# Performance work log

Hardware: AMD Instinct MI355X
Metric: run time of the kernel (lower is better)

Reference implementation:

```python
import jax, jax.numpy as jnp
import numpy as np

CAD = 5          # cubes_around_atoms_dim (default)
RES = 1.0        # resolution (default)
SIGMA = 0.93     # gaussian sigma from Li et al. 2014
LATO = 2 * CAD + 1


def _cube_offsets():
    # (LATO^3, 3) integer offsets of the neighborhood cube, as float32
    g = jnp.arange(-CAD, CAD + 1, dtype=jnp.float32)
    return jnp.stack(jnp.meshgrid(g, g, g, indexing='ij'), axis=-1).reshape(-1, 3)


def _compute_boxsize(coords):
    # Mirrors the torch code's data-dependent box sizing (concrete values).
    c = np.asarray(coords)
    minm = np.trunc(c.min(axis=1) / RES).min(axis=0)   # (3,)
    maxc = c.reshape(-1, 3).max(axis=0)                # (3,)
    return tuple(int(np.ceil(maxc[d] / RES) - minm[d] + (2 * CAD + 1)) for d in range(3))


def _forward(coords, radius, channels, numberchannels, boxsize):
    B, N, _ = coords.shape
    cube = _cube_offsets()                                   # (K,3), K = LATO^3
    mincoords = jnp.trunc(jnp.min(coords, axis=1) / RES)     # (B,3)
    translation = (mincoords - CAD)[:, None, :]              # (B,1,3)
    coords_s = coords * (1.0 / RES) - translation            # (B,N,3) scaled coords
    radius_s = radius * (1.0 / RES)                          # (B,N)
    # torch uses coords_scaled.data -> detached discrete coordinates
    disc = jnp.trunc(jax.lax.stop_gradient(coords_s))        # (B,N,3)
    # voxel centers: disc + cube + 1 + 0.5*resolution
    centers = disc[:, :, None, :] + cube[None, None] + (1.0 + 0.5 * RES)  # (B,N,K,3)
    dist = jnp.linalg.norm(coords_s[:, :, None, :] - centers, axis=-1)    # (B,N,K)
    expo = -(dist ** 2) / (SIGMA ** 2 * radius_s[:, :, None] ** 2)
    # torch clamps exponent at 10 via masked_fill (never hit: expo <= 0)
    occ = jnp.exp(jnp.minimum(expo, 10.0))                   # (B,N,K)
    idx = (disc[:, :, None, :] + cube[None, None] + 1.0).astype(jnp.int32)  # (B,N,K,3)
    b_idx = jnp.broadcast_to(jnp.arange(B, dtype=jnp.int32)[:, None, None], occ.shape)
    c_idx = jnp.broadcast_to(channels[:, :, None].astype(jnp.int32), occ.shape)
    vol = jnp.zeros((B, numberchannels) + boxsize, dtype=coords.dtype)
    vol = vol.at[b_idx.ravel(), c_idx.ravel(),
                 idx[..., 0].ravel(), idx[..., 1].ravel(), idx[..., 2].ravel()].add(occ.ravel())
    return vol


def setup_inputs() -> dict:
    key = jax.random.key(0)
    k1, k2, k3 = jax.random.split(key, 3)
    B, N, C = 4, 6000, 8
    coords = jax.random.uniform(k1, (B, N, 3), dtype=jnp.float32) * 60.0   # Angstrom box
    radius = 1.2 + 0.8 * jax.random.uniform(k2, (B, N), dtype=jnp.float32)  # vdW-like radii
    channels = jax.random.randint(k3, (B, N), 0, C)
    return {"coords": coords, "radius": radius, "channels": channels, "numberchannels": C}


def reference(coords, radius, channels, numberchannels):
    boxsize = _compute_boxsize(coords)
    return _forward(coords, radius, channels, numberchannels, boxsize)
```

## Files before the change

### kernel.cpp

```cpp
#include <hip/hip_runtime.h>


#define CAD 5
#define LATO 11
#define KOFF 1331
#define SIGMA 0.93f
#define BFIX 4
#define CFIX 8

#define RX 8
#define RY 8
#define RZ 8
#define XSTR 65
#define XCH_C (8 * XSTR)
#define STAGE 256
#define NBB_CAP 8192

#define WS_MIN   0
#define WS_MAX   12
#define WS_OFFS  48
#define WS_PACK  (WS_OFFS + BFIX * NBB_CAP + 64)

struct Geo {
    int bx, by, bz, nbx, nby, nbz, nbb, nrx, nry, nrz;
    float tr[BFIX][3];
};

__device__ __forceinline__ void derive_geo(const float* __restrict__ ws, Geo& g) {
    float box[3];
#pragma unroll
    for (int d = 0; d < 3; ++d) {
        float lo = 1e30f, hi = -1e30f;
#pragma unroll
        for (int b = 0; b < BFIX; ++b) {
            float mnb = truncf(ws[WS_MIN + b * 3 + d]);
            lo = fminf(lo, mnb);
            hi = fmaxf(hi, ws[WS_MAX + b * 3 + d]);
            g.tr[b][d] = mnb - (float)CAD;
        }
        box[d] = ceilf(hi) - lo + (float)(2 * CAD + 1);
    }
    g.bx = (int)box[0]; g.by = (int)box[1]; g.bz = (int)box[2];
    g.nbx = (g.bx + 3) >> 2; g.nby = (g.by + 3) >> 2; g.nbz = (g.bz + 3) >> 2;
    g.nbb = g.nbx * g.nby * g.nbz;
    g.nrx = (g.bx + RX - 1) / RX;
    g.nry = (g.by + RY - 1) / RY;
    g.nrz = (g.bz + RZ - 1) / RZ;
}

__global__ __launch_bounds__(256) void vx_minmax(const float* __restrict__ coords,
                                                 int N, float* __restrict__ ws) {
    int b = blockIdx.x;
    const float* c = coords + (size_t)b * N * 3;
    float mn[3] = {1e30f, 1e30f, 1e30f};
    float mx[3] = {-1e30f, -1e30f, -1e30f};
    for (int i = threadIdx.x; i < N; i += 256) {
#pragma unroll
        for (int d = 0; d < 3; ++d) {
            float v = c[i * 3 + d];
            mn[d] = fminf(mn[d], v);
            mx[d] = fmaxf(mx[d], v);
        }
    }
#pragma unroll
    for (int off = 32; off >= 1; off >>= 1) {
#pragma unroll
        for (int d = 0; d < 3; ++d) {
            mn[d] = fminf(mn[d], __shfl_down(mn[d], off, 64));
            mx[d] = fmaxf(mx[d], __shfl_down(mx[d], off, 64));
        }
    }
    __shared__ float smn[4][3], smx[4][3];
    int wave = threadIdx.x >> 6;
    if ((threadIdx.x & 63) == 0) {
#pragma unroll
        for (int d = 0; d < 3; ++d) { smn[wave][d] = mn[d]; smx[wave][d] = mx[d]; }
    }
    __syncthreads();
    if (threadIdx.x == 0) {
#pragma unroll
        for (int d = 0; d < 3; ++d) {
            for (int w = 1; w < 4; ++w) {
                mn[d] = fminf(mn[d], smn[w][d]);
                mx[d] = fmaxf(mx[d], smx[w][d]);
            }
            ws[WS_MIN + b * 3 + d] = mn[d];
            ws[WS_MAX + b * 3 + d] = mx[d];
        }
    }
}

__global__ __launch_bounds__(1024) void vx_bin(const float* __restrict__ coords,
                                               const float* __restrict__ radius,
                                               const int* __restrict__ channels,
                                               float* __restrict__ ws, int N) {
    int b = blockIdx.x;
    Geo g;
    derive_geo(ws, g);
    int* wsI = (int*)ws;
    int nbb = g.nbb;
    int t = threadIdx.x;

    __shared__ int cnt[NBB_CAP];
    __shared__ int ssum[1024];

    for (int i = t; i < nbb; i += 1024) cnt[i] = 0;
    __syncthreads();

    const float* cb = coords + (size_t)b * N * 3;
    float trx = g.tr[b][0], try_ = g.tr[b][1], trz = g.tr[b][2];

    for (int i = t; i < N; i += 1024) {
        float sx = cb[i * 3 + 0] - trx;
        float sy = cb[i * 3 + 1] - try_;
        float sz = cb[i * 3 + 2] - trz;
        int bin = ((((int)sx) >> 2) * g.nby + (((int)sy) >> 2)) * g.nbz + (((int)sz) >> 2);
        atomicAdd(&cnt[bin], 1);
    }
    __syncthreads();

    int base = t * 8;
    int v[8];
    int sum = 0;
#pragma unroll
    for (int k = 0; k < 8; ++k) {
        v[k] = sum;
        int idx = base + k;
        sum += (idx < nbb) ? cnt[idx] : 0;
    }
    ssum[t] = sum;
    __syncthreads();
    for (int off = 1; off < 1024; off <<= 1) {
        int x = (t >= off) ? ssum[t - off] : 0;
        __syncthreads();
        ssum[t] += x;
        __syncthreads();
    }
    int excl = ssum[t] - sum;
    int gbase = b * N;
#pragma unroll
    for (int k = 0; k < 8; ++k) {
        int idx = base + k;
        if (idx < nbb) {
            int off = gbase + excl + v[k];
            wsI[WS_OFFS + b * nbb + idx] = off;
        }
    }
    __syncthreads();
#pragma unroll
    for (int k = 0; k < 8; ++k) {
        int idx = base + k;
        if (idx < nbb) cnt[idx] = gbase + excl + v[k];
    }
    if (b == BFIX - 1 && t == 0) wsI[WS_OFFS + BFIX * nbb] = BFIX * N;
    __syncthreads();

    float4* p4 = (float4*)(ws + WS_PACK);
    for (int i = t; i < N; i += 1024) {
        float sx = cb[i * 3 + 0] - trx;
        float sy = cb[i * 3 + 1] - try_;
        float sz = cb[i * 3 + 2] - trz;
        int bin = ((((int)sx) >> 2) * g.nby + (((int)sy) >> 2)) * g.nbz + (((int)sz) >> 2);
        int pos = atomicAdd(&cnt[bin], 1);
        float r_ = radius[(size_t)b * N + i];
        float inv = -1.4426950408889634f / (SIGMA * SIGMA * r_ * r_);
        int ib = (__float_as_int(inv) & 0xFFFFFFF8) | (channels[(size_t)b * N + i] & 7);
        p4[pos] = make_float4(sx - 0.5f, sy - 0.5f, sz - 0.5f, __int_as_float(ib));
    }
}

#define ACC2(c) { a##c##_0 += e0; a##c##_1 += e1; }

#define BODY(A)                                                               \
    {                                                                         \
        float ddz = A.z - fzs;                                                \
        if (fabsf(ddz + 0.5f) <= 6.5f) {                                      \
            int ib = __float_as_int(A.w);                                     \
            int chs = __builtin_amdgcn_readfirstlane(ib & 7);                 \
            float inv = __int_as_float(ib & 0xFFFFFFF8);                      \
            float ddx = A.x - fvx;                                            \
            float ddy = A.y - fvy;                                            \
            float s2 = __builtin_fmaf(ddx, ddx, ddy * ddy);                   \
            float e0 =                                                        \
                __builtin_amdgcn_exp2f(__builtin_fmaf(ddz, ddz, s2) * inv);   \
            ddz -= 1.f;                                                       \
            float e1 =                                                        \
                __builtin_amdgcn_exp2f(__builtin_fmaf(ddz, ddz, s2) * inv);   \
            if (chs < 4) {                                                    \
                if (chs < 2) { if (chs == 0) ACC2(0) else ACC2(1) }           \
                else         { if (chs == 2) ACC2(2) else ACC2(3) }           \
            } else {                                                          \
                if (chs < 6) { if (chs == 4) ACC2(4) else ACC2(5) }           \
                else         { if (chs == 6) ACC2(6) else ACC2(7) }           \
            }                                                                 \
        }                                                                     \
    }

#define XW(c, s) \
    xch[(s) * XCH_C + (2 * wave + 0) * XSTR + lyx] = a##c##_0;                \
    xch[(s) * XCH_C + (2 * wave + 1) * XSTR + lyx] = a##c##_1;

__global__ __launch_bounds__(256) void vx_gather(
    const float* __restrict__ ws, float* __restrict__ out) {
    Geo g;
    derive_geo(ws, g);
    const int* wsI = (const int*)ws;
    const float4* __restrict__ pk4 = (const float4*)(ws + WS_PACK);
    int nreg = g.nrx * g.nry * g.nrz;
    int b = blockIdx.y;
    int t = threadIdx.x;
    int wave = t >> 6, lane = t & 63;
    int lx = lane >> 3, ly = lane & 7;
    int lyx = ly * 8 + lx;

    __shared__ float4 sA[STAGE];
    __shared__ float xch[4 * XCH_C];
    __shared__ int s_beg[32], s_roff[33];

    for (int reg = blockIdx.x; reg < nreg; reg += gridDim.x) {
        int rz = reg % g.nrz;
        int tmp = reg / g.nrz;
        int ry = tmp % g.nry;
        int rx = tmp / g.nry;
        int X0 = rx * RX, Y0 = ry * RY, Z0 = rz * RZ;
        int zs = Z0 + 2 * wave;

        float fvx = (float)(X0 + lx);
        float fvy = (float)(Y0 + ly);
        float fzs = (float)zs;

        float a0_0 = 0.f, a0_1 = 0.f, a1_0 = 0.f, a1_1 = 0.f;
        float a2_0 = 0.f, a2_1 = 0.f, a3_0 = 0.f, a3_1 = 0.f;
        float a4_0 = 0.f, a4_1 = 0.f, a5_0 = 0.f, a5_1 = 0.f;
        float a6_0 = 0.f, a6_1 = 0.f, a7_0 = 0.f, a7_1 = 0.f;

        int xb0 = max((X0 - 6) >> 2, 0), xb1 = min((X0 + RX + 3) >> 2, g.nbx - 1);
        int yb0 = max((Y0 - 6) >> 2, 0), yb1 = min((Y0 + RY + 3) >> 2, g.nby - 1);
        int zb0 = max((Z0 - 6) >> 2, 0), zb1 = min((Z0 + RZ + 3) >> 2, g.nbz - 1);
        int nyr = yb1 - yb0 + 1;
        int ncol = (xb1 - xb0 + 1) * nyr;

        if (t < 64) {
            int len = 0, beg = 0;
            if (t < ncol) {
                int xb = xb0 + t / nyr, yb = yb0 + t % nyr;
                int rb = b * g.nbb + (xb * g.nby + yb) * g.nbz;
                beg = wsI[WS_OFFS + rb + zb0];
                len = wsI[WS_OFFS + rb + zb1 + 1] - beg;
            }
            int incl = len;
#pragma unroll
            for (int off = 1; off < 32; off <<= 1) {
                int v = __shfl_up(incl, off, 64);
                if (t >= off) incl += v;
            }
            if (t < ncol) {
                s_beg[t] = beg;
                s_roff[t + 1] = incl;
            }
            if (t == 0) s_roff[0] = 0;
        }
        __syncthreads();
        int S = s_roff[ncol];

        for (int cb = 0; cb < S; cb += STAGE) {
            int cnt = min(STAGE, S - cb);
            if (t < cnt) {
                int gidx = cb + t;
                int r = 0;
                while (s_roff[r + 1] <= gidx) ++r;
                sA[t] = pk4[s_beg[r] + (gidx - s_roff[r])];
            }
            __syncthreads();
            int j = 0;
            for (; j + 3 < cnt; j += 4) {
                float4 A0 = sA[j];
                float4 A1 = sA[j + 1];
                float4 A2 = sA[j + 2];
                float4 A3 = sA[j + 3];
                BODY(A0) BODY(A1) BODY(A2) BODY(A3)
            }
            for (; j < cnt; ++j) {
                float4 A = sA[j];
                BODY(A)
            }
            __syncthreads();
        }

        bool interior = (X0 + RX <= g.bx) && (Y0 + RY <= g.by) && (Z0 + RZ <= g.bz);
#pragma unroll
        for (int half = 0; half < 2; ++half) {
            if (half == 0) { XW(0, 0) XW(1, 1) XW(2, 2) XW(3, 3) }
            else           { XW(4, 0) XW(5, 1) XW(6, 2) XW(7, 3) }
            __syncthreads();
            if (interior) {
#pragma unroll
                for (int k = 0; k < 8; ++k) {
                    int i = k * 256 + t;
                    int z = i & 7, y = (i >> 3) & 7, x = (i >> 6) & 7;
                    int c = (i >> 9) + half * 4;
                    out[(((size_t)(b * CFIX + c) * g.bx + X0 + x) * g.by + (Y0 + y)) *
                            (size_t)g.bz + Z0 + z] =
                        xch[(i >> 9) * XCH_C + z * XSTR + y * 8 + x];
                }
            } else {
#pragma unroll
                for (int k = 0; k < 8; ++k) {
                    int i = k * 256 + t;
                    int z = i & 7, y = (i >> 3) & 7, x = (i >> 6) & 7;
                    int c = (i >> 9) + half * 4;
                    if (X0 + x < g.bx && Y0 + y < g.by && Z0 + z < g.bz)
                        out[(((size_t)(b * CFIX + c) * g.bx + X0 + x) * g.by +
                             (Y0 + y)) * (size_t)g.bz + Z0 + z] =
                            xch[(i >> 9) * XCH_C + z * XSTR + y * 8 + x];
                }
            }
            __syncthreads();
        }
    }
}

__global__ __launch_bounds__(64) void vx_scatter(
    const float* __restrict__ coords, const float* __restrict__ radius,
    const int* __restrict__ channels, const int* __restrict__ nchan,
    const float* __restrict__ ws, int B, int N, float* __restrict__ out) {
    int atom = blockIdx.x;
    int b = atom / N;
    int lane = threadIdx.x;
    Geo g;
    derive_geo(ws, g);
    int C = *nchan;
    int bx = g.bx, by = g.by, bz = g.bz;

    float cx = coords[(size_t)atom * 3 + 0] - g.tr[b][0];
    float cy = coords[(size_t)atom * 3 + 1] - g.tr[b][1];
    float cz = coords[(size_t)atom * 3 + 2] - g.tr[b][2];
    float r = radius[atom];
    int ch = channels[atom];

    float dxf = truncf(cx), dyf = truncf(cy), dzf = truncf(cz);
    float fx = cx - dxf, fy = cy - dyf, fz = cz - dzf;
    int ix0 = (int)dxf - CAD + 1, iy0 = (int)dyf - CAD + 1, iz0 = (int)dzf - CAD + 1;
    float inv_s = 1.0f / (SIGMA * SIGMA * r * r);

    __shared__ float gg[3 * LATO];
    if (lane < 3 * LATO) {
        int dim = lane / LATO;
        int i = lane - dim * LATO;
        float f = (dim == 0) ? fx : (dim == 1 ? fy : fz);
        float d = f + ((float)CAD - 1.5f) - (float)i;
        gg[lane] = __expf(-d * d * inv_s);
    }
    __syncthreads();

    int base = (((b * C + ch) * bx + ix0) * by + iy0) * bz + iz0;
    int bybz = by * bz;
    for (int k = lane; k < KOFF; k += 64) {
        int i = k / (LATO * LATO);
        int rem = k - i * (LATO * LATO);
        int j = rem / LATO;
        int l = rem - j * LATO;
        float occ = gg[i] * gg[LATO + j] * gg[2 * LATO + l];
        atomicAdd(out + base + i * bybz + j * bz + l, occ);
    }
}

extern "C" void kernel_launch(void* const* d_in, const int* in_sizes, int n_in,
                              void* d_out, int out_size, void* d_ws, size_t ws_size,
                              hipStream_t stream) {
    const float* coords = (const float*)d_in[0];
    const float* radius = (const float*)d_in[1];
    const int* channels = (const int*)d_in[2];
    const int* nchan = (const int*)d_in[3];
    float* out = (float*)d_out;
    float* ws = (float*)d_ws;

    const int B = BFIX;
    int N = in_sizes[0] / (B * 3);
    size_t need = ((size_t)WS_PACK + (size_t)B * N * 4) * 4;

    vx_minmax<<<B, 256, 0, stream>>>(coords, N, ws);

    if (ws_size >= need) {
        vx_bin<<<B, 1024, 0, stream>>>(coords, radius, channels, ws, N);
        vx_gather<<<dim3(729, B), 256, 0, stream>>>(ws, out);
    } else {
        hipMemsetAsync(d_out, 0, (size_t)out_size * sizeof(float), stream);
        vx_scatter<<<B * N, 64, 0, stream>>>(coords, radius, channels, nchan, ws, B, N, out);
    }
}
```

Baseline: 102.1 us.

## Restructure gather kernel to one wave per region with eight z-voxels per thread

```diff
diff --git a/kernel.cpp b/kernel.cpp
--- a/kernel.cpp
+++ b/kernel.cpp
@@ -11,9 +11,7 @@
 #define RX 8
 #define RY 8
 #define RZ 8
-#define XSTR 65
-#define XCH_C (8 * XSTR)
-#define STAGE 256
+#define SAMAX 512
 #define NBB_CAP 8192
 
 #define WS_MIN   0
@@ -141,10 +139,7 @@
 #pragma unroll
     for (int k = 0; k < 8; ++k) {
         int idx = base + k;
-        if (idx < nbb) {
-            int off = gbase + excl + v[k];
-            wsI[WS_OFFS + b * nbb + idx] = off;
-        }
+        if (idx < nbb) wsI[WS_OFFS + b * nbb + idx] = gbase + excl + v[k];
     }
     __syncthreads();
 #pragma unroll
@@ -169,38 +164,70 @@
     }
 }
 
-#define ACC2(c) { a##c##_0 += e0; a##c##_1 += e1; }
-
-#define BODY(A)                                                               \
+#define DECL8(c)                                                              \
+    float a##c##_0 = 0.f, a##c##_1 = 0.f, a##c##_2 = 0.f, a##c##_3 = 0.f,     \
+          a##c##_4 = 0.f, a##c##_5 = 0.f, a##c##_6 = 0.f, a##c##_7 = 0.f;
+
+#define ACC8(c)                                                               \
+    { a##c##_0 += e0; a##c##_1 += e1; a##c##_2 += e2; a##c##_3 += e3;         \
+      a##c##_4 += e4; a##c##_5 += e5; a##c##_6 += e6; a##c##_7 += e7; }
+
+#define BODY8(A)                                                              \
     {                                                                         \
-        float ddz = A.z - fzs;                                                \
-        if (fabsf(ddz + 0.5f) <= 6.5f) {                                      \
-            int ib = __float_as_int(A.w);                                     \
-            int chs = __builtin_amdgcn_readfirstlane(ib & 7);                 \
-            float inv = __int_as_float(ib & 0xFFFFFFF8);                      \
-            float ddx = A.x - fvx;                                            \
-            float ddy = A.y - fvy;                                            \
-            float s2 = __builtin_fmaf(ddx, ddx, ddy * ddy);                   \
-            float e0 =                                                        \
-                __builtin_amdgcn_exp2f(__builtin_fmaf(ddz, ddz, s2) * inv);   \
-            ddz -= 1.f;                                                       \
-            float e1 =                                                        \
-                __builtin_amdgcn_exp2f(__builtin_fmaf(ddz, ddz, s2) * inv);   \
-            if (chs < 4) {                                                    \
-                if (chs < 2) { if (chs == 0) ACC2(0) else ACC2(1) }           \
-                else         { if (chs == 2) ACC2(2) else ACC2(3) }           \
-            } else {                                                          \
-                if (chs < 6) { if (chs == 4) ACC2(4) else ACC2(5) }           \
-                else         { if (chs == 6) ACC2(6) else ACC2(7) }           \
-            }                                                                 \
+        int ib = __float_as_int(A.w);                                         \
+        int chs = __builtin_amdgcn_readfirstlane(ib & 7);                     \
+        float inv = __int_as_float(ib & 0xFFFFFFF8);                          \
+        float ddx = A.x - fvx;                                                \
+        float ddy = A.y - fvy;                                                \
+        float s2 = __builtin_fmaf(ddx, ddx, ddy * ddy);                       \
+        float dz = A.z - fZ0;                                                 \
+        float e0 = __builtin_amdgcn_exp2f(__builtin_fmaf(dz, dz, s2) * inv);  \
+        dz -= 1.f;                                                            \
+        float e1 = __builtin_amdgcn_exp2f(__builtin_fmaf(dz, dz, s2) * inv);  \
+        dz -= 1.f;                                                            \
+        float e2 = __builtin_amdgcn_exp2f(__builtin_fmaf(dz, dz, s2) * inv);  \
+        dz -= 1.f;                                                            \
+        float e3 = __builtin_amdgcn_exp2f(__builtin_fmaf(dz, dz, s2) * inv);  \
+        dz -= 1.f;                                                            \
+        float e4 = __builtin_amdgcn_exp2f(__builtin_fmaf(dz, dz, s2) * inv);  \
+        dz -= 1.f;                                                            \
+        float e5 = __builtin_amdgcn_exp2f(__builtin_fmaf(dz, dz, s2) * inv);  \
+        dz -= 1.f;                                                            \
+        float e6 = __builtin_amdgcn_exp2f(__builtin_fmaf(dz, dz, s2) * inv);  \
+        dz -= 1.f;                                                            \
+        float e7 = __builtin_amdgcn_exp2f(__builtin_fmaf(dz, dz, s2) * inv);  \
+        if (chs < 4) {                                                        \
+            if (chs < 2) { if (chs == 0) ACC8(0) else ACC8(1) }               \
+            else         { if (chs == 2) ACC8(2) else ACC8(3) }               \
+        } else {                                                              \
+            if (chs < 6) { if (chs == 4) ACC8(4) else ACC8(5) }               \
+            else         { if (chs == 6) ACC8(6) else ACC8(7) }               \
         }                                                                     \
     }
 
-#define XW(c, s) \
-    xch[(s) * XCH_C + (2 * wave + 0) * XSTR + lyx] = a##c##_0;                \
-    xch[(s) * XCH_C + (2 * wave + 1) * XSTR + lyx] = a##c##_1;
-
-__global__ __launch_bounds__(256) void vx_gather(
+#define STORE8(c)                                                             \
+    if (okxy) {                                                               \
+        size_t basec =                                                        \
+            (((size_t)(b * CFIX + c) * g.bx + vxv) * g.by + vyv) *            \
+                (size_t)g.bz + Z0;                                            \
+        if (nz == 8) {                                                        \
+            out[basec + 0] = a##c##_0; out[basec + 1] = a##c##_1;             \
+            out[basec + 2] = a##c##_2; out[basec + 3] = a##c##_3;             \
+            out[basec + 4] = a##c##_4; out[basec + 5] = a##c##_5;             \
+            out[basec + 6] = a##c##_6; out[basec + 7] = a##c##_7;             \
+        } else {                                                              \
+            if (0 < nz) out[basec + 0] = a##c##_0;                            \
+            if (1 < nz) out[basec + 1] = a##c##_1;                            \
+            if (2 < nz) out[basec + 2] = a##c##_2;                            \
+            if (3 < nz) out[basec + 3] = a##c##_3;                            \
+            if (4 < nz) out[basec + 4] = a##c##_4;                            \
+            if (5 < nz) out[basec + 5] = a##c##_5;                            \
+            if (6 < nz) out[basec + 6] = a##c##_6;                            \
+            if (7 < nz) out[basec + 7] = a##c##_7;                            \
+        }                                                                     \
+    }
+
+__global__ __launch_bounds__(64, 3) void vx_gather(
     const float* __restrict__ ws, float* __restrict__ out) {
     Geo g;
     derive_geo(ws, g);
@@ -209,13 +236,10 @@
     int nreg = g.nrx * g.nry * g.nrz;
     int b = blockIdx.y;
     int t = threadIdx.x;
-    int wave = t >> 6, lane = t & 63;
-    int lx = lane >> 3, ly = lane & 7;
-    int lyx = ly * 8 + lx;
-
-    __shared__ float4 sA[STAGE];
-    __shared__ float xch[4 * XCH_C];
-    __shared__ int s_beg[32], s_roff[33];
+    int lx = t >> 3, ly = t & 7;
+
+    __shared__ float4 sA[SAMAX];
+    __shared__ int s_beg[64], s_roff[65];
 
     for (int reg = blockIdx.x; reg < nreg; reg += gridDim.x) {
         int rz = reg % g.nrz;
@@ -223,100 +247,88 @@
         int ry = tmp % g.nry;
         int rx = tmp / g.nry;
         int X0 = rx * RX, Y0 = ry * RY, Z0 = rz * RZ;
-        int zs = Z0 + 2 * wave;
 
         float fvx = (float)(X0 + lx);
         float fvy = (float)(Y0 + ly);
-        float fzs = (float)zs;
-
-        float a0_0 = 0.f, a0_1 = 0.f, a1_0 = 0.f, a1_1 = 0.f;
-        float a2_0 = 0.f, a2_1 = 0.f, a3_0 = 0.f, a3_1 = 0.f;
-        float a4_0 = 0.f, a4_1 = 0.f, a5_0 = 0.f, a5_1 = 0.f;
-        float a6_0 = 0.f, a6_1 = 0.f, a7_0 = 0.f, a7_1 = 0.f;
-
-        int xb0 = max((X0 - 6) >> 2, 0), xb1 = min((X0 + RX + 3) >> 2, g.nbx - 1);
-        int yb0 = max((Y0 - 6) >> 2, 0), yb1 = min((Y0 + RY + 3) >> 2, g.nby - 1);
-        int zb0 = max((Z0 - 6) >> 2, 0), zb1 = min((Z0 + RZ + 3) >> 2, g.nbz - 1);
+        float fZ0 = (float)Z0;
+
+        DECL8(0) DECL8(1) DECL8(2) DECL8(3)
+        DECL8(4) DECL8(5) DECL8(6) DECL8(7)
+
+        int xb0 = max((X0 - 6) >> 2, 0), xb1 = min((X0 + 11) >> 2, g.nbx - 1);
+        int yb0 = max((Y0 - 6) >> 2, 0), yb1 = min((Y0 + 11) >> 2, g.nby - 1);
+        int zb0 = max((Z0 - 6) >> 2, 0), zb1 = min((Z0 + 11) >> 2, g.nbz - 1);
         int nyr = yb1 - yb0 + 1;
         int ncol = (xb1 - xb0 + 1) * nyr;
 
-        if (t < 64) {
-            int len = 0, beg = 0;
-            if (t < ncol) {
-                int xb = xb0 + t / nyr, yb = yb0 + t % nyr;
-                int rb = b * g.nbb + (xb * g.nby + yb) * g.nbz;
-                beg = wsI[WS_OFFS + rb + zb0];
-                len = wsI[WS_OFFS + rb + zb1 + 1] - beg;
-            }
-            int incl = len;
-#pragma unroll
-            for (int off = 1; off < 32; off <<= 1) {
-                int v = __shfl_up(incl, off, 64);
-                if (t >= off) incl += v;
-            }
-            if (t < ncol) {
-                s_beg[t] = beg;
-                s_roff[t + 1] = incl;
-            }
-            if (t == 0) s_roff[0] = 0;
-        }
-        __syncthreads();
-        int S = s_roff[ncol];
-
-        for (int cb = 0; cb < S; cb += STAGE) {
-            int cnt = min(STAGE, S - cb);
-            if (t < cnt) {
-                int gidx = cb + t;
-                int r = 0;
-                while (s_roff[r + 1] <= gidx) ++r;
-                sA[t] = pk4[s_beg[r] + (gidx - s_roff[r])];
+        int len = 0, beg = 0;
+        if (t < ncol) {
+            int xb = xb0 + t / nyr, yb = yb0 + t % nyr;
+            int rb = b * g.nbb + (xb * g.nby + yb) * g.nbz;
+            beg = wsI[WS_OFFS + rb + zb0];
+            len = wsI[WS_OFFS + rb + zb1 + 1] - beg;
+        }
+        int incl = len;
+#pragma unroll
+        for (int off = 1; off < 64; off <<= 1) {
+            int v = __shfl_up(incl, off, 64);
+            if (t >= off) incl += v;
+        }
+        int excl = incl - len;
+        int S = __shfl(incl, 63, 64);
+
+        if (S <= SAMAX) {
+            int col = t >> 1, slot = t & 1;
+            int beg_c = __shfl(beg, col, 64);
+            int ro_c = __shfl(excl, col, 64);
+            int len_c = __shfl(len, col, 64);
+            if (col < ncol) {
+                for (int e = slot; e < len_c; e += 2)
+                    sA[ro_c + e] = pk4[beg_c + e];
             }
             __syncthreads();
             int j = 0;
-            for (; j + 3 < cnt; j += 4) {
+            for (; j + 3 < S; j += 4) {
                 float4 A0 = sA[j];
                 float4 A1 = sA[j + 1];
                 float4 A2 = sA[j + 2];
                 float4 A3 = sA[j + 3];
-                BODY(A0) BODY(A1) BODY(A2) BODY(A3)
-            }
-            for (; j < cnt; ++j) {
+                BODY8(A0) BODY8(A1) BODY8(A2) BODY8(A3)
+            }
+            for (; j < S; ++j) {
                 float4 A = sA[j];
-                BODY(A)
+                BODY8(A)
             }
             __syncthreads();
-        }
-
-        bool interior = (X0 + RX <= g.bx) && (Y0 + RY <= g.by) && (Z0 + RZ <= g.bz);
-#pragma unroll
-        for (int half = 0; half < 2; ++half) {
-            if (half == 0) { XW(0, 0) XW(1, 1) XW(2, 2) XW(3, 3) }
-            else           { XW(4, 0) XW(5, 1) XW(6, 2) XW(7, 3) }
+        } else {
+            if (t < ncol) {
+                s_beg[t] = beg;
+                s_roff[t + 1] = incl;
+            }
+            if (t == 0) s_roff[0] = 0;
             __syncthreads();
-            if (interior) {
-#pragma unroll
-                for (int k = 0; k < 8; ++k) {
-                    int i = k * 256 + t;
-                    int z = i & 7, y = (i >> 3) & 7, x = (i >> 6) & 7;
-                    int c = (i >> 9) + half * 4;
-                    out[(((size_t)(b * CFIX + c) * g.bx + X0 + x) * g.by + (Y0 + y)) *
-                            (size_t)g.bz + Z0 + z] =
-                        xch[(i >> 9) * XCH_C + z * XSTR + y * 8 + x];
+            for (int cb2 = 0; cb2 < S; cb2 += 64) {
+                int cnt = min(64, S - cb2);
+                if (t < cnt) {
+                    int gidx = cb2 + t;
+                    int r = 0;
+                    while (s_roff[r + 1] <= gidx) ++r;
+                    sA[t] = pk4[s_beg[r] + (gidx - s_roff[r])];
                 }
-            } else {
-#pragma unroll
-                for (int k = 0; k < 8; ++k) {
-                    int i = k * 256 + t;
-                    int z = i & 7, y = (i >> 3) & 7, x = (i >> 6) & 7;
-                    int c = (i >> 9) + half * 4;
-                    if (X0 + x < g.bx && Y0 + y < g.by && Z0 + z < g.bz)
-                        out[(((size_t)(b * CFIX + c) * g.bx + X0 + x) * g.by +
-                             (Y0 + y)) * (size_t)g.bz + Z0 + z] =
-                            xch[(i >> 9) * XCH_C + z * XSTR + y * 8 + x];
+                __syncthreads();
+                for (int j = 0; j < cnt; ++j) {
+                    float4 A = sA[j];
+                    BODY8(A)
                 }
-            }
-            __syncthreads();
-        }
+                __syncthreads();
+            }
+        }
+
+        int vxv = X0 + lx, vyv = Y0 + ly;
+        bool okxy = (vxv < g.bx) && (vyv < g.by);
+        int nz = min(8, g.bz - Z0);
+        STORE8(0) STORE8(1) STORE8(2) STORE8(3)
+        STORE8(4) STORE8(5) STORE8(6) STORE8(7)
     }
 }
 
@@ -383,7 +395,7 @@
 
     if (ws_size >= need) {
         vx_bin<<<B, 1024, 0, stream>>>(coords, radius, channels, ws, N);
-        vx_gather<<<dim3(729, B), 256, 0, stream>>>(ws, out);
+        vx_gather<<<dim3(768, B), 64, 0, stream>>>(ws, out);
     } else {
         hipMemsetAsync(d_out, 0, (size_t)out_size * sizeof(float), stream);
         vx_scatter<<<B * N, 64, 0, stream>>>(coords, radius, channels, nchan, ws, B, N, out);
```

New measurement: 115.5 us. +13.2%, slower.

## Bin atoms by channel so gather sweeps each channel without per-atom branching

Applied to the files above, without the earlier changes.

```diff
diff --git a/kernel.cpp b/kernel.cpp
--- a/kernel.cpp
+++ b/kernel.cpp
@@ -13,13 +13,16 @@
 #define RZ 8
 #define XSTR 65
 #define XCH_C (8 * XSTR)
-#define STAGE 256
-#define NBB_CAP 8192
+#define SAMAX 512
+#define NBB_CAP 6144
+#define KEYCAP (NBB_CAP * CFIX)
+#define KPT (KEYCAP / 1024)
 
 #define WS_MIN   0
 #define WS_MAX   12
 #define WS_OFFS  48
-#define WS_PACK  (WS_OFFS + BFIX * NBB_CAP + 64)
+#define WS_CUR   (WS_OFFS + BFIX * KEYCAP + 64)
+#define WS_PACK  (WS_CUR + BFIX * KEYCAP + 64)
 
 struct Geo {
     int bx, by, bz, nbx, nby, nbz, nbb, nrx, nry, nrz;
@@ -89,6 +92,8 @@
         }
     }
 }
+
+#define GETC(k) ((cntp[(k) >> 1] >> (((k) & 1) * 16)) & 0xFFFFu)
 
 __global__ __launch_bounds__(1024) void vx_bin(const float* __restrict__ coords,
                                                const float* __restrict__ radius,
@@ -98,13 +103,13 @@
     Geo g;
     derive_geo(ws, g);
     int* wsI = (int*)ws;
-    int nbb = g.nbb;
+    int nbb8 = g.nbb * CFIX;
     int t = threadIdx.x;
 
-    __shared__ int cnt[NBB_CAP];
+    __shared__ unsigned int cntp[KEYCAP / 2];
     __shared__ int ssum[1024];
 
-    for (int i = t; i < nbb; i += 1024) cnt[i] = 0;
+    for (int i = t; i < KEYCAP / 2; i += 1024) cntp[i] = 0u;
     __syncthreads();
 
     const float* cb = coords + (size_t)b * N * 3;
@@ -114,19 +119,19 @@
         float sx = cb[i * 3 + 0] - trx;
         float sy = cb[i * 3 + 1] - try_;
         float sz = cb[i * 3 + 2] - trz;
-        int bin = ((((int)sx) >> 2) * g.nby + (((int)sy) >> 2)) * g.nbz + (((int)sz) >> 2);
-        atomicAdd(&cnt[bin], 1);
-    }
-    __syncthreads();
-
-    int base = t * 8;
-    int v[8];
+        int ch = channels[(size_t)b * N + i] & 7;
+        int key = (((((int)sx) >> 2) * g.nby + (((int)sy) >> 2)) * CFIX + ch) * g.nbz +
+                  (((int)sz) >> 2);
+        atomicAdd(&cntp[key >> 1], 1u << ((key & 1) * 16));
+    }
+    __syncthreads();
+
+    int base = t * KPT;
     int sum = 0;
 #pragma unroll
-    for (int k = 0; k < 8; ++k) {
-        v[k] = sum;
+    for (int k = 0; k < KPT; ++k) {
         int idx = base + k;
-        sum += (idx < nbb) ? cnt[idx] : 0;
+        if (idx < nbb8) sum += (int)GETC(idx);
     }
     ssum[t] = sum;
     __syncthreads();
@@ -136,23 +141,17 @@
         ssum[t] += x;
         __syncthreads();
     }
-    int excl = ssum[t] - sum;
-    int gbase = b * N;
-#pragma unroll
-    for (int k = 0; k < 8; ++k) {
+    int run = b * N + ssum[t] - sum;
+#pragma unroll
+    for (int k = 0; k < KPT; ++k) {
         int idx = base + k;
-        if (idx < nbb) {
-            int off = gbase + excl + v[k];
-            wsI[WS_OFFS + b * nbb + idx] = off;
-        }
-    }
-    __syncthreads();
-#pragma unroll
-    for (int k = 0; k < 8; ++k) {
-        int idx = base + k;
-        if (idx < nbb) cnt[idx] = gbase + excl + v[k];
-    }
-    if (b == BFIX - 1 && t == 0) wsI[WS_OFFS + BFIX * nbb] = BFIX * N;
+        if (idx < nbb8) {
+            wsI[WS_OFFS + b * nbb8 + idx] = run;
+            wsI[WS_CUR + b * nbb8 + idx] = run;
+            run += (int)GETC(idx);
+        }
+    }
+    if (b == BFIX - 1 && t == 0) wsI[WS_OFFS + BFIX * nbb8] = BFIX * N;
     __syncthreads();
 
     float4* p4 = (float4*)(ws + WS_PACK);
@@ -160,43 +159,47 @@
         float sx = cb[i * 3 + 0] - trx;
         float sy = cb[i * 3 + 1] - try_;
         float sz = cb[i * 3 + 2] - trz;
-        int bin = ((((int)sx) >> 2) * g.nby + (((int)sy) >> 2)) * g.nbz + (((int)sz) >> 2);
-        int pos = atomicAdd(&cnt[bin], 1);
+        int ch = channels[(size_t)b * N + i] & 7;
+        int key = (((((int)sx) >> 2) * g.nby + (((int)sy) >> 2)) * CFIX + ch) * g.nbz +
+                  (((int)sz) >> 2);
+        int pos = atomicAdd(&wsI[WS_CUR + b * nbb8 + key], 1);
         float r_ = radius[(size_t)b * N + i];
         float inv = -1.4426950408889634f / (SIGMA * SIGMA * r_ * r_);
-        int ib = (__float_as_int(inv) & 0xFFFFFFF8) | (channels[(size_t)b * N + i] & 7);
-        p4[pos] = make_float4(sx - 0.5f, sy - 0.5f, sz - 0.5f, __int_as_float(ib));
-    }
-}
-
+        p4[pos] = make_float4(sx - 0.5f, sy - 0.5f, sz - 0.5f, inv);
+    }
+}
+
+#define DECL2(c) float a##c##_0 = 0.f, a##c##_1 = 0.f;
 #define ACC2(c) { a##c##_0 += e0; a##c##_1 += e1; }
 
-#define BODY(A)                                                               \
+#define BODYF(A, c)                                                           \
     {                                                                         \
         float ddz = A.z - fzs;                                                \
         if (fabsf(ddz + 0.5f) <= 6.5f) {                                      \
-            int ib = __float_as_int(A.w);                                     \
-            int chs = __builtin_amdgcn_readfirstlane(ib & 7);                 \
-            float inv = __int_as_float(ib & 0xFFFFFFF8);                      \
             float ddx = A.x - fvx;                                            \
             float ddy = A.y - fvy;                                            \
             float s2 = __builtin_fmaf(ddx, ddx, ddy * ddy);                   \
             float e0 =                                                        \
-                __builtin_amdgcn_exp2f(__builtin_fmaf(ddz, ddz, s2) * inv);   \
+                __builtin_amdgcn_exp2f(__builtin_fmaf(ddz, ddz, s2) * A.w);   \
             ddz -= 1.f;                                                       \
             float e1 =                                                        \
-                __builtin_amdgcn_exp2f(__builtin_fmaf(ddz, ddz, s2) * inv);   \
-            if (chs < 4) {                                                    \
-                if (chs < 2) { if (chs == 0) ACC2(0) else ACC2(1) }           \
-                else         { if (chs == 2) ACC2(2) else ACC2(3) }           \
-            } else {                                                          \
-                if (chs < 6) { if (chs == 4) ACC2(4) else ACC2(5) }           \
-                else         { if (chs == 6) ACC2(6) else ACC2(7) }           \
-            }                                                                 \
+                __builtin_amdgcn_exp2f(__builtin_fmaf(ddz, ddz, s2) * A.w);   \
+            ACC2(c)                                                           \
         }                                                                     \
     }
 
-#define XW(c, s) \
+#define SWEEP_CH(c)                                                           \
+    {                                                                         \
+        int jb = s_roff[(c) * ncolxy], je = s_roff[((c) + 1) * ncolxy];       \
+        int j = jb;                                                           \
+        for (; j + 3 < je; j += 4) {                                          \
+            float4 A0 = sA[j], A1 = sA[j + 1], A2 = sA[j + 2], A3 = sA[j + 3];\
+            BODYF(A0, c) BODYF(A1, c) BODYF(A2, c) BODYF(A3, c)               \
+        }                                                                     \
+        for (; j < je; ++j) { float4 A = sA[j]; BODYF(A, c) }                 \
+    }
+
+#define XW(c, s)                                                              \
     xch[(s) * XCH_C + (2 * wave + 0) * XSTR + lyx] = a##c##_0;                \
     xch[(s) * XCH_C + (2 * wave + 1) * XSTR + lyx] = a##c##_1;
 
@@ -206,6 +209,7 @@
     derive_geo(ws, g);
     const int* wsI = (const int*)ws;
     const float4* __restrict__ pk4 = (const float4*)(ws + WS_PACK);
+    int nbb8 = g.nbb * CFIX;
     int nreg = g.nrx * g.nry * g.nrz;
     int b = blockIdx.y;
     int t = threadIdx.x;
@@ -213,9 +217,10 @@
     int lx = lane >> 3, ly = lane & 7;
     int lyx = ly * 8 + lx;
 
-    __shared__ float4 sA[STAGE];
+    __shared__ float4 sA[SAMAX];
     __shared__ float xch[4 * XCH_C];
-    __shared__ int s_beg[32], s_roff[33];
+    __shared__ int s_beg[208], s_roff[208];
+    __shared__ int wtot[4];
 
     for (int reg = blockIdx.x; reg < nreg; reg += gridDim.x) {
         int rz = reg % g.nrz;
@@ -229,63 +234,83 @@
         float fvy = (float)(Y0 + ly);
         float fzs = (float)zs;
 
-        float a0_0 = 0.f, a0_1 = 0.f, a1_0 = 0.f, a1_1 = 0.f;
-        float a2_0 = 0.f, a2_1 = 0.f, a3_0 = 0.f, a3_1 = 0.f;
-        float a4_0 = 0.f, a4_1 = 0.f, a5_0 = 0.f, a5_1 = 0.f;
-        float a6_0 = 0.f, a6_1 = 0.f, a7_0 = 0.f, a7_1 = 0.f;
-
-        int xb0 = max((X0 - 6) >> 2, 0), xb1 = min((X0 + RX + 3) >> 2, g.nbx - 1);
-        int yb0 = max((Y0 - 6) >> 2, 0), yb1 = min((Y0 + RY + 3) >> 2, g.nby - 1);
-        int zb0 = max((Z0 - 6) >> 2, 0), zb1 = min((Z0 + RZ + 3) >> 2, g.nbz - 1);
+        DECL2(0) DECL2(1) DECL2(2) DECL2(3)
+        DECL2(4) DECL2(5) DECL2(6) DECL2(7)
+
+        int xb0 = max((X0 - 6) >> 2, 0), xb1 = min((X0 + 11) >> 2, g.nbx - 1);
+        int yb0 = max((Y0 - 6) >> 2, 0), yb1 = min((Y0 + 11) >> 2, g.nby - 1);
+        int zb0 = max((Z0 - 6) >> 2, 0), zb1 = min((Z0 + 11) >> 2, g.nbz - 1);
         int nyr = yb1 - yb0 + 1;
-        int ncol = (xb1 - xb0 + 1) * nyr;
-
-        if (t < 64) {
-            int len = 0, beg = 0;
-            if (t < ncol) {
-                int xb = xb0 + t / nyr, yb = yb0 + t % nyr;
-                int rb = b * g.nbb + (xb * g.nby + yb) * g.nbz;
-                beg = wsI[WS_OFFS + rb + zb0];
-                len = wsI[WS_OFFS + rb + zb1 + 1] - beg;
-            }
-            int incl = len;
-#pragma unroll
-            for (int off = 1; off < 32; off <<= 1) {
-                int v = __shfl_up(incl, off, 64);
-                if (t >= off) incl += v;
-            }
-            if (t < ncol) {
-                s_beg[t] = beg;
-                s_roff[t + 1] = incl;
-            }
-            if (t == 0) s_roff[0] = 0;
-        }
+        int ncolxy = (xb1 - xb0 + 1) * nyr;
+        int NR = ncolxy * CFIX;
+
+        int len = 0, beg = 0;
+        if (t < NR) {
+            int ch = t / ncolxy;
+            int col = t - ch * ncolxy;
+            int xb = xb0 + col / nyr, yb = yb0 + col % nyr;
+            int keyb = ((xb * g.nby + yb) * CFIX + ch) * g.nbz;
+            beg = wsI[WS_OFFS + b * nbb8 + keyb + zb0];
+            len = wsI[WS_OFFS + b * nbb8 + keyb + zb1 + 1] - beg;
+        }
+        int incl = len;
+#pragma unroll
+        for (int off = 1; off < 64; off <<= 1) {
+            int v = __shfl_up(incl, off, 64);
+            if (lane >= off) incl += v;
+        }
+        if (lane == 63) wtot[wave] = incl;
         __syncthreads();
-        int S = s_roff[ncol];
-
-        for (int cb = 0; cb < S; cb += STAGE) {
-            int cnt = min(STAGE, S - cb);
-            if (t < cnt) {
-                int gidx = cb + t;
-                int r = 0;
-                while (s_roff[r + 1] <= gidx) ++r;
-                sA[t] = pk4[s_beg[r] + (gidx - s_roff[r])];
+        int addb = 0;
+        for (int w = 0; w < 4; ++w)
+            if (w < wave) addb += wtot[w];
+        incl += addb;
+        int excl = incl - len;
+        if (t < NR) {
+            s_beg[t] = beg;
+            s_roff[t + 1] = incl;
+        }
+        if (t == 0) s_roff[0] = 0;
+        __syncthreads();
+        int S = s_roff[NR];
+
+        if (S <= SAMAX) {
+            if (t < NR) {
+                for (int e = 0; e < len; ++e)
+                    sA[excl + e] = pk4[beg + e];
             }
             __syncthreads();
-            int j = 0;
-            for (; j + 3 < cnt; j += 4) {
-                float4 A0 = sA[j];
-                float4 A1 = sA[j + 1];
-                float4 A2 = sA[j + 2];
-                float4 A3 = sA[j + 3];
-                BODY(A0) BODY(A1) BODY(A2) BODY(A3)
+            SWEEP_CH(0) SWEEP_CH(1) SWEEP_CH(2) SWEEP_CH(3)
+            SWEEP_CH(4) SWEEP_CH(5) SWEEP_CH(6) SWEEP_CH(7)
+        } else {
+            __syncthreads();
+            for (int r2 = 0; r2 < NR; ++r2) {
+                int bg = s_beg[r2];
+                int ln = s_roff[r2 + 1] - s_roff[r2];
+                int c = r2 / ncolxy;
+                for (int e = 0; e < ln; ++e) {
+                    float4 A = pk4[bg + e];
+                    float ddz = A.z - fzs;
+                    if (fabsf(ddz + 0.5f) <= 6.5f) {
+                        float ddx = A.x - fvx, ddy = A.y - fvy;
+                        float s2 = __builtin_fmaf(ddx, ddx, ddy * ddy);
+                        float e0 = __builtin_amdgcn_exp2f(
+                            __builtin_fmaf(ddz, ddz, s2) * A.w);
+                        ddz -= 1.f;
+                        float e1 = __builtin_amdgcn_exp2f(
+                            __builtin_fmaf(ddz, ddz, s2) * A.w);
+                        if (c < 4) {
+                            if (c < 2) { if (c == 0) ACC2(0) else ACC2(1) }
+                            else       { if (c == 2) ACC2(2) else ACC2(3) }
+                        } else {
+                            if (c < 6) { if (c == 4) ACC2(4) else ACC2(5) }
+                            else       { if (c == 6) ACC2(6) else ACC2(7) }
+                        }
+                    }
+                }
             }
-            for (; j < cnt; ++j) {
-                float4 A = sA[j];
-                BODY(A)
-            }
-            __syncthreads();
-        }
+        }
+        __syncthreads();
 
         bool interior = (X0 + RX <= g.bx) && (Y0 + RY <= g.by) && (Z0 + RZ <= g.bz);
 #pragma unroll
```

Result: slower. 142.2 us (+39.3%).
